# Kernel tuning notes

Hardware: AMD Instinct MI355X
Metric: run time of the kernel (lower is better)

The kernel has to match this reference:

```python
import jax, jax.numpy as jnp
import numpy as np

D_MODEL = 1024
NUM_HEADS = 16
BATCH = 4
SEQ = 2048


def _trunc_normal(key, shape, std):
    # truncated normal in [-3*std, 3*std], matching nn.init.trunc_normal_
    return jax.random.truncated_normal(key, -3.0, 3.0, shape, dtype=jnp.float32) * std


def setup_inputs() -> dict:
    key = jax.random.key(0)
    kx, kq, kk, kv, ko = jax.random.split(key, 5)
    std = np.sqrt(2.0 / (D_MODEL + D_MODEL)).astype(np.float32)
    x = jax.random.normal(kx, (BATCH, SEQ, D_MODEL), dtype=jnp.float32)
    # nn.Linear stores weight as [out, in]; y = x @ W.T
    W_q = _trunc_normal(kq, (D_MODEL, D_MODEL), std)
    W_k = _trunc_normal(kk, (D_MODEL, D_MODEL), std)
    W_v = _trunc_normal(kv, (D_MODEL, D_MODEL), std)
    W_o = _trunc_normal(ko, (D_MODEL, D_MODEL), std)
    return {"x": x, "W_q": W_q, "W_k": W_k, "W_v": W_v, "W_o": W_o}


def reference(x, W_q, W_k, W_v, W_o):
    b, s, d_model = x.shape
    h = NUM_HEADS
    d_k = d_model // h

    def split_heads(t):
        return t.reshape(b, s, h, d_k).transpose(0, 2, 1, 3)  # b h s d

    Q = split_heads(x @ W_q.T)
    K = split_heads(x @ W_k.T)
    V = split_heads(x @ W_v.T)

    # F.scaled_dot_product_attention with attn_mask=None -> NON-causal
    scale = 1.0 / jnp.sqrt(jnp.asarray(d_k, dtype=x.dtype))
    scores = jnp.einsum('bhqd,bhkd->bhqk', Q, K) * scale
    attn = jax.nn.softmax(scores, axis=-1)
    out = jnp.einsum('bhqk,bhkd->bhqd', attn, V)
    out = out.transpose(0, 2, 1, 3).reshape(b, s, d_model)
    return out @ W_o.T
```

## Files before the change

### kernel.cpp

```cpp
#include <hip/hip_runtime.h>
#include <hip/hip_bf16.h>
#include <stdint.h>


#define D_MODEL 1024
#define NHEAD 16
#define BATCH 4
#define SEQ 2048
#define DK 64
#define MTOT (BATCH * SEQ)

typedef __attribute__((ext_vector_type(4))) float f32x4;
typedef __attribute__((ext_vector_type(16))) float f32x16;
typedef __attribute__((ext_vector_type(8))) __bf16 bf16x8;
typedef __attribute__((ext_vector_type(8))) unsigned short ushort8;
typedef __attribute__((ext_vector_type(4))) unsigned short us4;

static __device__ __forceinline__ unsigned short f2bf(float f) {
  union { float f; unsigned int u; } v;
  v.f = f;
  unsigned int r = v.u + (0x7fffu + ((v.u >> 16) & 1u));
  return (unsigned short)(r >> 16);
}

static __device__ __forceinline__ f32x4 mfma16(bf16x8 a, bf16x8 b, f32x4 c) {
  return __builtin_amdgcn_mfma_f32_16x16x32_bf16(a, b, c, 0, 0, 0);
}
static __device__ __forceinline__ f32x16 mfma32(bf16x8 a, bf16x8 b, f32x16 c) {
  return __builtin_amdgcn_mfma_f32_32x32x16_bf16(a, b, c, 0, 0, 0);
}

static __device__ __forceinline__ unsigned int cvt_pk_bf16(float lo, float hi) {
  unsigned int r;
  asm("v_cvt_pk_bf16_f32 %0, %1, %2" : "=v"(r) : "v"(lo), "v"(hi));
  return r;
}

static __device__ __forceinline__ void gl_lds16(const void* g, void* l) {
  __builtin_amdgcn_global_load_lds((const __attribute__((address_space(1))) void*)g,
                                   (__attribute__((address_space(3))) void*)l, 16, 0, 0);
}

__global__ __launch_bounds__(256) void cvt_f32_bf16(const float* __restrict__ in,
                                                    unsigned short* __restrict__ out) {
  int i = blockIdx.x * 256 + threadIdx.x;
  f32x4 a = ((const f32x4*)in)[2 * i];
  f32x4 b = ((const f32x4*)in)[2 * i + 1];
  ushort8 r;
  r[0] = f2bf(a[0]); r[1] = f2bf(a[1]); r[2] = f2bf(a[2]); r[3] = f2bf(a[3]);
  r[4] = f2bf(b[0]); r[5] = f2bf(b[1]); r[6] = f2bf(b[2]); r[7] = f2bf(b[3]);
  ((ushort8*)out)[i] = r;
}

__global__ __launch_bounds__(256, 2) void gemm_qkv(const unsigned short* __restrict__ A,
                                                   const unsigned short* __restrict__ B3,
                                                   unsigned short* __restrict__ qh,
                                                   unsigned short* __restrict__ kh,
                                                   unsigned short* __restrict__ vtg,
                                                   float qscale) {
  __shared__ unsigned short lA[128][64];
  __shared__ unsigned short lB[128][64];
  const int t = threadIdx.x;
  const int wid = t >> 6, lane = t & 63;
  const int lr = lane & 15, lg = lane >> 4;
  const int wr = wid >> 1, wc = wid & 1;
  const int m0 = blockIdx.y * 128, n0 = blockIdx.x * 128;
  const int row8 = t >> 3, c8 = t & 7;

  f32x4 acc[4][4] = {};

  for (int kt = 0; kt < 16; ++kt) {
    const int k0 = kt * 64;
    if (kt) __syncthreads();
#pragma unroll
    for (int p = 0; p < 4; ++p) {
      gl_lds16(A  + (size_t)(m0 + p * 32 + row8) * 1024 + k0 + c8 * 8,
               &lA[0][0] + p * 2048 + t * 8);
      gl_lds16(B3 + (size_t)(n0 + p * 32 + row8) * 1024 + k0 + c8 * 8,
               &lB[0][0] + p * 2048 + t * 8);
    }
    __syncthreads();

    bf16x8 af[4][2], bfr[4][2];
#pragma unroll
    for (int rb = 0; rb < 4; ++rb)
#pragma unroll
      for (int kb = 0; kb < 2; ++kb) {
        af[rb][kb] = *(const bf16x8*)&lA[wr * 64 + rb * 16 + lr][kb * 32 + lg * 8];
        bfr[rb][kb] = *(const bf16x8*)&lB[wc * 64 + rb * 16 + lr][kb * 32 + lg * 8];
      }
    __builtin_amdgcn_s_setprio(1);
#pragma unroll
    for (int rb = 0; rb < 4; ++rb)
#pragma unroll
      for (int cb = 0; cb < 4; ++cb)
#pragma unroll
        for (int kb = 0; kb < 2; ++kb)
          acc[rb][cb] = mfma16(af[rb][kb], bfr[cb][kb], acc[rb][cb]);
    __builtin_amdgcn_s_setprio(0);
  }

  const int sel = n0 >> 10;
  const float scale = (sel == 0) ? qscale : 1.0f;
#pragma unroll
  for (int rb = 0; rb < 4; ++rb) {
    int mbase = m0 + wr * 64 + rb * 16 + lg * 4;
    int b = mbase >> 11, s0 = mbase & 2047;
#pragma unroll
    for (int cb = 0; cb < 4; ++cb) {
      int n = n0 + wc * 64 + cb * 16 + lr;
      int nl = n & 1023;
      int h = nl >> 6, d = nl & 63;
      if (sel == 2) {
        us4 v;
#pragma unroll
        for (int j = 0; j < 4; ++j) v[j] = f2bf(acc[rb][cb][j]);
        *(us4*)(vtg + ((size_t)(b * NHEAD + h) * DK + d) * SEQ + s0) = v;
      } else {
        unsigned short* out = (sel == 0) ? qh : kh;
#pragma unroll
        for (int j = 0; j < 4; ++j)
          out[((size_t)(b * NHEAD + h) * SEQ + s0 + j) * DK + d] = f2bf(acc[rb][cb][j] * scale);
      }
    }
  }
}

__global__ __launch_bounds__(256, 2) void gemm_o(const unsigned short* __restrict__ A,
                                                 const unsigned short* __restrict__ B,
                                                 float* __restrict__ out) {
  __shared__ unsigned short lA[128][64];
  __shared__ unsigned short lB[128][64];
  const int t = threadIdx.x;
  const int wid = t >> 6, lane = t & 63;
  const int lr = lane & 15, lg = lane >> 4;
  const int wr = wid >> 1, wc = wid & 1;
  const int m0 = blockIdx.y * 128, n0 = blockIdx.x * 128;
  const int row8 = t >> 3, c8 = t & 7;

  f32x4 acc[4][4] = {};

  for (int kt = 0; kt < 16; ++kt) {
    const int k0 = kt * 64;
    if (kt) __syncthreads();
#pragma unroll
    for (int p = 0; p < 4; ++p) {
      gl_lds16(A + (size_t)(m0 + p * 32 + row8) * 1024 + k0 + c8 * 8,
               &lA[0][0] + p * 2048 + t * 8);
      gl_lds16(B + (size_t)(n0 + p * 32 + row8) * 1024 + k0 + c8 * 8,
               &lB[0][0] + p * 2048 + t * 8);
    }
    __syncthreads();

    bf16x8 af[4][2], bfr[4][2];
#pragma unroll
    for (int rb = 0; rb < 4; ++rb)
#pragma unroll
      for (int kb = 0; kb < 2; ++kb) {
        af[rb][kb] = *(const bf16x8*)&lA[wr * 64 + rb * 16 + lr][kb * 32 + lg * 8];
        bfr[rb][kb] = *(const bf16x8*)&lB[wc * 64 + rb * 16 + lr][kb * 32 + lg * 8];
      }
    __builtin_amdgcn_s_setprio(1);
#pragma unroll
    for (int rb = 0; rb < 4; ++rb)
#pragma unroll
      for (int cb = 0; cb < 4; ++cb)
#pragma unroll
        for (int kb = 0; kb < 2; ++kb)
          acc[rb][cb] = mfma16(af[rb][kb], bfr[cb][kb], acc[rb][cb]);
    __builtin_amdgcn_s_setprio(0);
  }

#pragma unroll
  for (int rb = 0; rb < 4; ++rb) {
    int mbase = m0 + wr * 64 + rb * 16 + lg * 4;
#pragma unroll
    for (int cb = 0; cb < 4; ++cb) {
      int n = n0 + wc * 64 + cb * 16 + lr;
#pragma unroll
      for (int j = 0; j < 4; ++j)
        out[(size_t)(mbase + j) * 1024 + n] = acc[rb][cb][j];
    }
  }
}

__global__ __launch_bounds__(256, 2) void attn_fwd(const unsigned short* __restrict__ Qh,
                                                   const unsigned short* __restrict__ Kh,
                                                   const unsigned short* __restrict__ Vt_g,
                                                   unsigned short* __restrict__ Oout) {
  __shared__ unsigned short Kl[64 * 64];
  __shared__ unsigned short Vl[64 * 64];

  const int t = threadIdx.x;
  const int wq = t >> 6, lane = t & 63;
  const int l31 = lane & 31, hi = lane >> 5;

  const int wg = blockIdx.x;
  const int work = (wg & 7) * 64 + (wg >> 3);
  const int bh = work >> 3, qi = work & 7;
  const int q0 = qi * 256 + wq * 64;
  const size_t base = (size_t)bh * SEQ * DK;
  const int srow = t >> 3, sc = t & 7;

  bf16x8 qf0[4], qf1[4];
#pragma unroll
  for (int dt = 0; dt < 4; ++dt) {
    qf0[dt] = *(const bf16x8*)(Qh + base + (size_t)(q0 + l31) * DK + dt * 16 + hi * 8);
    qf1[dt] = *(const bf16x8*)(Qh + base + (size_t)(q0 + 32 + l31) * DK + dt * 16 + hi * 8);
  }

  f32x16 o0[2] = {}, o1[2] = {};
  float l0 = 0.f, l1 = 0.f;

  ushort8 rk0 = *(const ushort8*)(Kh + base + (size_t)srow * DK + sc * 8);
  ushort8 rk1 = *(const ushort8*)(Kh + base + (size_t)(srow + 32) * DK + sc * 8);
  ushort8 rv0 = *(const ushort8*)(Vt_g + base + (size_t)srow * SEQ + sc * 8);
  ushort8 rv1 = *(const ushort8*)(Vt_g + base + (size_t)(srow + 32) * SEQ + sc * 8);

  for (int kt = 0; kt < SEQ / 64; ++kt) {
    __syncthreads();
    {
      const int r0 = srow, r1 = srow + 32;
      *(ushort8*)((char*)Kl + ((r0 * 128 + sc * 16) ^ ((r0 & 7) << 4))) = rk0;
      *(ushort8*)((char*)Kl + ((r1 * 128 + sc * 16) ^ ((r1 & 7) << 4))) = rk1;
      *(ushort8*)((char*)Vl + ((r0 * 128 + sc * 16) ^ ((r0 & 7) << 4))) = rv0;
      *(ushort8*)((char*)Vl + ((r1 * 128 + sc * 16) ^ ((r1 & 7) << 4))) = rv1;
    }
    __syncthreads();

    if (kt < SEQ / 64 - 1) {
      const int nxt = (kt + 1) * 64;
      rk0 = *(const ushort8*)(Kh + base + (size_t)(nxt + srow) * DK + sc * 8);
      rk1 = *(const ushort8*)(Kh + base + (size_t)(nxt + srow + 32) * DK + sc * 8);
      rv0 = *(const ushort8*)(Vt_g + base + (size_t)srow * SEQ + nxt + sc * 8);
      rv1 = *(const ushort8*)(Vt_g + base + (size_t)(srow + 32) * SEQ + nxt + sc * 8);
    }

    f32x16 sS0[2] = {}, sS1[2] = {};
    __builtin_amdgcn_s_setprio(1);
#pragma unroll
    for (int kb = 0; kb < 2; ++kb) {
      const int row = kb * 32 + l31;
#pragma unroll
      for (int dt = 0; dt < 4; ++dt) {
        bf16x8 kf = *(const bf16x8*)((const char*)Kl +
                      ((row * 128 + dt * 32 + hi * 16) ^ ((row & 7) << 4)));
        sS0[kb] = mfma32(kf, qf0[dt], sS0[kb]);
        sS1[kb] = mfma32(kf, qf1[dt], sS1[kb]);
      }
    }
    __builtin_amdgcn_s_setprio(0);

    {
      float a0 = 0.f, a1 = 0.f, a2 = 0.f, a3 = 0.f;
#pragma unroll
      for (int kb = 0; kb < 2; ++kb)
#pragma unroll
        for (int r = 0; r < 16; r += 4) {
          float p0 = __builtin_amdgcn_exp2f(sS0[kb][r + 0]);
          float p1 = __builtin_amdgcn_exp2f(sS0[kb][r + 1]);
          float p2 = __builtin_amdgcn_exp2f(sS0[kb][r + 2]);
          float p3 = __builtin_amdgcn_exp2f(sS0[kb][r + 3]);
          sS0[kb][r + 0] = p0; sS0[kb][r + 1] = p1;
          sS0[kb][r + 2] = p2; sS0[kb][r + 3] = p3;
          a0 += p0; a1 += p1; a2 += p2; a3 += p3;
        }
      float ps = (a0 + a1) + (a2 + a3);
      ps += __shfl_xor(ps, 32, 64);
      l0 += ps;
    }
    {
      float a0 = 0.f, a1 = 0.f, a2 = 0.f, a3 = 0.f;
#pragma unroll
      for (int kb = 0; kb < 2; ++kb)
#pragma unroll
        for (int r = 0; r < 16; r += 4) {
          float p0 = __builtin_amdgcn_exp2f(sS1[kb][r + 0]);
          float p1 = __builtin_amdgcn_exp2f(sS1[kb][r + 1]);
          float p2 = __builtin_amdgcn_exp2f(sS1[kb][r + 2]);
          float p3 = __builtin_amdgcn_exp2f(sS1[kb][r + 3]);
          sS1[kb][r + 0] = p0; sS1[kb][r + 1] = p1;
          sS1[kb][r + 2] = p2; sS1[kb][r + 3] = p3;
          a0 += p0; a1 += p1; a2 += p2; a3 += p3;
        }
      float ps = (a0 + a1) + (a2 + a3);
      ps += __shfl_xor(ps, 32, 64);
      l1 += ps;
    }

    __builtin_amdgcn_s_setprio(1);
#pragma unroll
    for (int ks = 0; ks < 4; ++ks) {
      const int kk = ks >> 1, rb = (ks & 1) * 8;
      unsigned int a0 = cvt_pk_bf16(sS0[kk][rb + 0], sS0[kk][rb + 1]);
      unsigned int a1 = cvt_pk_bf16(sS0[kk][rb + 2], sS0[kk][rb + 3]);
      unsigned int b0 = cvt_pk_bf16(sS0[kk][rb + 4], sS0[kk][rb + 5]);
      unsigned int b1 = cvt_pk_bf16(sS0[kk][rb + 6], sS0[kk][rb + 7]);
      asm("v_permlane32_swap_b32 %0, %1" : "+v"(a0), "+v"(b0));
      asm("v_permlane32_swap_b32 %0, %1" : "+v"(a1), "+v"(b1));
      union { unsigned int u[4]; bf16x8 v; } pw0;
      pw0.u[0] = a0; pw0.u[1] = a1; pw0.u[2] = b0; pw0.u[3] = b1;

      unsigned int c0 = cvt_pk_bf16(sS1[kk][rb + 0], sS1[kk][rb + 1]);
      unsigned int c1 = cvt_pk_bf16(sS1[kk][rb + 2], sS1[kk][rb + 3]);
      unsigned int d0 = cvt_pk_bf16(sS1[kk][rb + 4], sS1[kk][rb + 5]);
      unsigned int d1 = cvt_pk_bf16(sS1[kk][rb + 6], sS1[kk][rb + 7]);
      asm("v_permlane32_swap_b32 %0, %1" : "+v"(c0), "+v"(d0));
      asm("v_permlane32_swap_b32 %0, %1" : "+v"(c1), "+v"(d1));
      union { unsigned int u[4]; bf16x8 v; } pw1;
      pw1.u[0] = c0; pw1.u[1] = c1; pw1.u[2] = d0; pw1.u[3] = d1;

#pragma unroll
      for (int dt = 0; dt < 2; ++dt) {
        const int row = dt * 32 + l31;
        bf16x8 vf = *(const bf16x8*)((const char*)Vl +
                      ((row * 128 + ks * 32 + hi * 16) ^ ((row & 7) << 4)));
        o0[dt] = mfma32(vf, pw0.v, o0[dt]);
        o1[dt] = mfma32(vf, pw1.v, o1[dt]);
      }
    }
    __builtin_amdgcn_s_setprio(0);
  }

  const int b = bh >> 4, hh = bh & 15;
  {
    const int q = q0 + l31;
    const float inv = 1.0f / l0;
    unsigned short* orow = Oout + (size_t)(b * SEQ + q) * D_MODEL + hh * 64 + hi * 4;
#pragma unroll
    for (int dt = 0; dt < 2; ++dt)
#pragma unroll
      for (int i = 0; i < 4; ++i) {
        us4 v;
#pragma unroll
        for (int j = 0; j < 4; ++j) v[j] = f2bf(o0[dt][4 * i + j] * inv);
        *(us4*)(orow + dt * 32 + 8 * i) = v;
      }
  }
  {
    const int q = q0 + 32 + l31;
    const float inv = 1.0f / l1;
    unsigned short* orow = Oout + (size_t)(b * SEQ + q) * D_MODEL + hh * 64 + hi * 4;
#pragma unroll
    for (int dt = 0; dt < 2; ++dt)
#pragma unroll
      for (int i = 0; i < 4; ++i) {
        us4 v;
#pragma unroll
        for (int j = 0; j < 4; ++j) v[j] = f2bf(o1[dt][4 * i + j] * inv);
        *(us4*)(orow + dt * 32 + 8 * i) = v;
      }
  }
}

extern "C" void kernel_launch(void* const* d_in, const int* in_sizes, int n_in,
                              void* d_out, int out_size, void* d_ws, size_t ws_size,
                              hipStream_t stream) {
  (void)in_sizes; (void)n_in; (void)out_size; (void)ws_size;
  const float* x = (const float*)d_in[0];
  const float* Wq = (const float*)d_in[1];
  const float* Wk = (const float*)d_in[2];
  const float* Wv = (const float*)d_in[3];
  const float* Wo = (const float*)d_in[4];

  char* ws = (char*)d_ws;
  unsigned short* xb   = (unsigned short*)(ws + 0);
  unsigned short* wqkv = (unsigned short*)(ws + 16777216);
  unsigned short* wob  = (unsigned short*)(ws + 23068672);
  unsigned short* qh   = (unsigned short*)(ws + 25165824);
  unsigned short* kh   = (unsigned short*)(ws + 41943040);
  unsigned short* vtg  = (unsigned short*)(ws + 58720256);
  unsigned short* at   = (unsigned short*)(ws + 75497472);

  cvt_f32_bf16<<<4096, 256, 0, stream>>>(x, xb);
  cvt_f32_bf16<<<512, 256, 0, stream>>>(Wq, wqkv);
  cvt_f32_bf16<<<512, 256, 0, stream>>>(Wk, wqkv + 1048576);
  cvt_f32_bf16<<<512, 256, 0, stream>>>(Wv, wqkv + 2097152);
  cvt_f32_bf16<<<512, 256, 0, stream>>>(Wo, wob);

  gemm_qkv<<<dim3(24, 64), 256, 0, stream>>>(xb, wqkv, qh, kh, vtg, 0.1803368801f);

  attn_fwd<<<512, 256, 0, stream>>>(qh, kh, vtg, at);

  gemm_o<<<dim3(8, 64), 256, 0, stream>>>(at, wob, (float*)d_out);
}
```

Measured before the change: 188.2 us.

## Split attention KV range into two halves with a merge kernel; fuse weight casts

The attention kernel now splits each (batch, head, query-block) job over two halves of the key/value sequence. That doubles the number of workgroups to 1024 and raises the occupancy hint to 4 waves. Each half writes an unnormalized bf16 partial output and its row sums, and a new merge kernel adds the two partials and normalizes by the combined sum. The four weight-conversion launches become one kernel, and the GEMM launch bounds rise to 3 blocks per CU. This adds extra HBM traffic for the partial outputs and the merge pass, adds bf16 rounding of the partials, and the tighter launch bounds risk register spills.

```diff
diff --git a/kernel.cpp b/kernel.cpp
--- a/kernel.cpp
+++ b/kernel.cpp
@@ -21,6 +21,11 @@
   v.f = f;
   unsigned int r = v.u + (0x7fffu + ((v.u >> 16) & 1u));
   return (unsigned short)(r >> 16);
+}
+static __device__ __forceinline__ float bf2f(unsigned short u) {
+  union { unsigned int u; float f; } v;
+  v.u = (unsigned int)u << 16;
+  return v.f;
 }
 
 static __device__ __forceinline__ f32x4 mfma16(bf16x8 a, bf16x8 b, f32x4 c) {
@@ -52,7 +57,23 @@
   ((ushort8*)out)[i] = r;
 }
 
-__global__ __launch_bounds__(256, 2) void gemm_qkv(const unsigned short* __restrict__ A,
+__global__ __launch_bounds__(256) void cvt_w4(const float* __restrict__ wq,
+                                              const float* __restrict__ wk,
+                                              const float* __restrict__ wv,
+                                              const float* __restrict__ wo,
+                                              unsigned short* __restrict__ out) {
+  const int sel = blockIdx.x >> 9;
+  const float* in = (sel == 0) ? wq : (sel == 1) ? wk : (sel == 2) ? wv : wo;
+  int i = (blockIdx.x & 511) * 256 + threadIdx.x;
+  f32x4 a = ((const f32x4*)in)[2 * i];
+  f32x4 b = ((const f32x4*)in)[2 * i + 1];
+  ushort8 r;
+  r[0] = f2bf(a[0]); r[1] = f2bf(a[1]); r[2] = f2bf(a[2]); r[3] = f2bf(a[3]);
+  r[4] = f2bf(b[0]); r[5] = f2bf(b[1]); r[6] = f2bf(b[2]); r[7] = f2bf(b[3]);
+  ((ushort8*)(out + (size_t)sel * 1048576))[i] = r;
+}
+
+__global__ __launch_bounds__(256, 3) void gemm_qkv(const unsigned short* __restrict__ A,
                                                    const unsigned short* __restrict__ B3,
                                                    unsigned short* __restrict__ qh,
                                                    unsigned short* __restrict__ kh,
@@ -126,7 +147,7 @@
   }
 }
 
-__global__ __launch_bounds__(256, 2) void gemm_o(const unsigned short* __restrict__ A,
+__global__ __launch_bounds__(256, 3) void gemm_o(const unsigned short* __restrict__ A,
                                                  const unsigned short* __restrict__ B,
                                                  float* __restrict__ out) {
   __shared__ unsigned short lA[128][64];
@@ -184,10 +205,12 @@
   }
 }
 
-__global__ __launch_bounds__(256, 2) void attn_fwd(const unsigned short* __restrict__ Qh,
+__global__ __launch_bounds__(256, 4) void attn_fwd(const unsigned short* __restrict__ Qh,
                                                    const unsigned short* __restrict__ Kh,
                                                    const unsigned short* __restrict__ Vt_g,
-                                                   unsigned short* __restrict__ Oout) {
+                                                   unsigned short* __restrict__ P0,
+                                                   unsigned short* __restrict__ P1,
+                                                   float* __restrict__ Lb) {
   __shared__ unsigned short Kl[64 * 64];
   __shared__ unsigned short Vl[64 * 64];
 
@@ -196,11 +219,14 @@
   const int l31 = lane & 31, hi = lane >> 5;
 
   const int wg = blockIdx.x;
-  const int work = (wg & 7) * 64 + (wg >> 3);
-  const int bh = work >> 3, qi = work & 7;
+  const int work = (wg & 7) * 128 + (wg >> 3);
+  const int half = work >> 9;
+  const int rem = work & 511;
+  const int bh = rem >> 3, qi = rem & 7;
   const int q0 = qi * 256 + wq * 64;
   const size_t base = (size_t)bh * SEQ * DK;
   const int srow = t >> 3, sc = t & 7;
+  const int kvbase = half * 1024;
 
   bf16x8 qf0[4], qf1[4];
 #pragma unroll
@@ -212,12 +238,12 @@
   f32x16 o0[2] = {}, o1[2] = {};
   float l0 = 0.f, l1 = 0.f;
 
-  ushort8 rk0 = *(const ushort8*)(Kh + base + (size_t)srow * DK + sc * 8);
-  ushort8 rk1 = *(const ushort8*)(Kh + base + (size_t)(srow + 32) * DK + sc * 8);
-  ushort8 rv0 = *(const ushort8*)(Vt_g + base + (size_t)srow * SEQ + sc * 8);
-  ushort8 rv1 = *(const ushort8*)(Vt_g + base + (size_t)(srow + 32) * SEQ + sc * 8);
-
-  for (int kt = 0; kt < SEQ / 64; ++kt) {
+  ushort8 rk0 = *(const ushort8*)(Kh + base + (size_t)(kvbase + srow) * DK + sc * 8);
+  ushort8 rk1 = *(const ushort8*)(Kh + base + (size_t)(kvbase + srow + 32) * DK + sc * 8);
+  ushort8 rv0 = *(const ushort8*)(Vt_g + base + (size_t)srow * SEQ + kvbase + sc * 8);
+  ushort8 rv1 = *(const ushort8*)(Vt_g + base + (size_t)(srow + 32) * SEQ + kvbase + sc * 8);
+
+  for (int kt = 0; kt < 16; ++kt) {
     __syncthreads();
     {
       const int r0 = srow, r1 = srow + 32;
@@ -228,8 +254,8 @@
     }
     __syncthreads();
 
-    if (kt < SEQ / 64 - 1) {
-      const int nxt = (kt + 1) * 64;
+    if (kt < 15) {
+      const int nxt = kvbase + (kt + 1) * 64;
       rk0 = *(const ushort8*)(Kh + base + (size_t)(nxt + srow) * DK + sc * 8);
       rk1 = *(const ushort8*)(Kh + base + (size_t)(nxt + srow + 32) * DK + sc * 8);
       rv0 = *(const ushort8*)(Vt_g + base + (size_t)srow * SEQ + nxt + sc * 8);
@@ -323,34 +349,53 @@
   }
 
   const int b = bh >> 4, hh = bh & 15;
+  unsigned short* pat = half ? P1 : P0;
   {
     const int q = q0 + l31;
-    const float inv = 1.0f / l0;
-    unsigned short* orow = Oout + (size_t)(b * SEQ + q) * D_MODEL + hh * 64 + hi * 4;
+    unsigned short* orow = pat + (size_t)(b * SEQ + q) * D_MODEL + hh * 64 + hi * 4;
 #pragma unroll
     for (int dt = 0; dt < 2; ++dt)
 #pragma unroll
       for (int i = 0; i < 4; ++i) {
         us4 v;
 #pragma unroll
-        for (int j = 0; j < 4; ++j) v[j] = f2bf(o0[dt][4 * i + j] * inv);
+        for (int j = 0; j < 4; ++j) v[j] = f2bf(o0[dt][4 * i + j]);
         *(us4*)(orow + dt * 32 + 8 * i) = v;
       }
+    if (hi == 0) Lb[(size_t)(half * 64 + bh) * SEQ + q] = l0;
   }
   {
     const int q = q0 + 32 + l31;
-    const float inv = 1.0f / l1;
-    unsigned short* orow = Oout + (size_t)(b * SEQ + q) * D_MODEL + hh * 64 + hi * 4;
+    unsigned short* orow = pat + (size_t)(b * SEQ + q) * D_MODEL + hh * 64 + hi * 4;
 #pragma unroll
     for (int dt = 0; dt < 2; ++dt)
 #pragma unroll
       for (int i = 0; i < 4; ++i) {
         us4 v;
 #pragma unroll
-        for (int j = 0; j < 4; ++j) v[j] = f2bf(o1[dt][4 * i + j] * inv);
+        for (int j = 0; j < 4; ++j) v[j] = f2bf(o1[dt][4 * i + j]);
         *(us4*)(orow + dt * 32 + 8 * i) = v;
       }
-  }
+    if (hi == 0) Lb[(size_t)(half * 64 + bh) * SEQ + q] = l1;
+  }
+}
+
+__global__ __launch_bounds__(256) void merge_halves(unsigned short* __restrict__ p0,
+                                                    const unsigned short* __restrict__ p1,
+                                                    const float* __restrict__ Lb) {
+  const int tid = blockIdx.x * 256 + threadIdx.x;
+  const size_t e = (size_t)tid * 8;
+  const int h = (int)((e >> 6) & 15);
+  const int s = (int)((e >> 10) & 2047);
+  const int b = (int)(e >> 21);
+  const size_t li = (size_t)(b * NHEAD + h) * SEQ + s;
+  const float inv = 1.0f / (Lb[li] + Lb[(size_t)64 * SEQ + li]);
+  ushort8 a = *(const ushort8*)(p0 + e);
+  ushort8 c = *(const ushort8*)(p1 + e);
+  ushort8 r;
+#pragma unroll
+  for (int j = 0; j < 8; ++j) r[j] = f2bf((bf2f(a[j]) + bf2f(c[j])) * inv);
+  *(ushort8*)(p0 + e) = r;
 }
 
 extern "C" void kernel_launch(void* const* d_in, const int* in_sizes, int n_in,
@@ -372,15 +417,16 @@
   unsigned short* vtg  = (unsigned short*)(ws + 58720256);
   unsigned short* at   = (unsigned short*)(ws + 75497472);
 
+  unsigned short* p1 = xb;
+  float* lb = (float*)wqkv;
+
   cvt_f32_bf16<<<4096, 256, 0, stream>>>(x, xb);
-  cvt_f32_bf16<<<512, 256, 0, stream>>>(Wq, wqkv);
-  cvt_f32_bf16<<<512, 256, 0, stream>>>(Wk, wqkv + 1048576);
-  cvt_f32_bf16<<<512, 256, 0, stream>>>(Wv, wqkv + 2097152);
-  cvt_f32_bf16<<<512, 256, 0, stream>>>(Wo, wob);
+  cvt_w4<<<2048, 256, 0, stream>>>(Wq, Wk, Wv, Wo, wqkv);
 
   gemm_qkv<<<dim3(24, 64), 256, 0, stream>>>(xb, wqkv, qh, kh, vtg, 0.1803368801f);
 
-  attn_fwd<<<512, 256, 0, stream>>>(qh, kh, vtg, at);
+  attn_fwd<<<1024, 256, 0, stream>>>(qh, kh, vtg, at, p1, lb);
+  merge_halves<<<4096, 256, 0, stream>>>(at, p1, lb);
 
   gemm_o<<<dim3(8, 64), 256, 0, stream>>>(at, wob, (float*)d_out);
 }
```

Measured after the change: 743.0 us. 295% more time.
